# Kernel optimization log

Hardware: AMD Instinct MI355X
Metric: run time of the kernel (lower is better)

The kernel has to match this reference:

```python
import jax, jax.numpy as jnp
import numpy as np

B, C, H, W = 8, 256, 64, 64

def setup_inputs() -> dict:
    key = jax.random.key(0)
    ks = jax.random.split(key, 8)
    s = 0.02  # keep logits in a sane range
    return {
        "x": jax.random.normal(ks[0], (B, C, H, W), jnp.float32),
        "motion_info": jax.random.normal(ks[1], (B, C, H, W), jnp.float32),
        "wq": jax.random.normal(ks[2], (C, C), jnp.float32) * s,
        "bq": jax.random.normal(ks[3], (C,), jnp.float32) * s,
        "wk": jax.random.normal(ks[4], (C, C), jnp.float32) * s,
        "bk": jax.random.normal(ks[5], (C,), jnp.float32) * s,
        "wv": jax.random.normal(ks[6], (C, C), jnp.float32) * s,
        "bv": jax.random.normal(ks[7], (C,), jnp.float32) * s,
    }

def reference(x, motion_info, wq, bq, wk, bk, wv, bv):
    b, c, h, w = x.shape
    n = h * w
    scale = c ** (-0.5)
    # 1x1 convs == channel-mixing GEMMs; flatten spatial to tokens
    xf = x.reshape(b, c, n)              # [B,C,N]
    mf = motion_info.reshape(b, c, n)    # [B,C,N]
    q = jnp.einsum('dc,bcn->bdn', wq, xf) + bq[None, :, None]
    k = jnp.einsum('dc,bcn->bdn', wk, mf) + bk[None, :, None]
    v = jnp.einsum('dc,bcn->bdn', wv, mf) + bv[None, :, None]
    # attn[b,i,j] = <q[:,i], k[:,j]> * scale, softmax over j
    attn = jax.nn.softmax(jnp.einsum('bci,bcj->bij', q, k) * scale, axis=-1)
    # out[b,c,i] = sum_j v[b,c,j] * attn[b,i,j]
    out = jnp.einsum('bcj,bij->bci', v, attn)
    return out.reshape(b, c, h, w)
```

## Files before the change

kernel.cpp:

```cpp
#include <hip/hip_runtime.h>
#include <hip/hip_bf16.h>

#define BATCH 8
#define CH    256
#define NTOK  4096

typedef __bf16 bf16_t;
typedef __bf16 bf16x8 __attribute__((ext_vector_type(8)));
typedef __bf16 bf16x4 __attribute__((ext_vector_type(4)));
typedef float  fx4    __attribute__((ext_vector_type(4)));

#define GLOAD_LDS16(gptr, lptr) \
    __builtin_amdgcn_global_load_lds( \
        (const __attribute__((address_space(1))) void*)(gptr), \
        (__attribute__((address_space(3))) void*)(lptr), 16, 0, 0)


__global__ __launch_bounds__(256, 2) void proj_kernel(
    const float* __restrict__ x, const float* __restrict__ motion,
    const float* __restrict__ wq, const float* __restrict__ bq,
    const float* __restrict__ wk, const float* __restrict__ bk,
    const float* __restrict__ wv, const float* __restrict__ bv,
    bf16_t* __restrict__ qg, bf16_t* __restrict__ kg, bf16_t* __restrict__ vg)
{
    const int mat = blockIdx.y;
    const int b   = blockIdx.x & 7;
    const int n0  = (blockIdx.x >> 3) * 64;
    const float* __restrict__ src  = (mat == 0) ? x  : motion;
    const float* __restrict__ W    = (mat == 0) ? wq : (mat == 1 ? wk : wv);
    const float* __restrict__ bias = (mat == 0) ? bq : (mat == 1 ? bk : bv);

    __shared__ __align__(16) unsigned char smem[55296 + 1024];
    bf16_t* Xt    = (bf16_t*)smem;
    bf16_t* Wl    = (bf16_t*)(smem + 33792);
    bf16_t* OutL  = (bf16_t*)smem;
    float*  biasL = (float*)(smem + 55296);

    const int tid  = threadIdx.x;
    const int w    = tid >> 6;
    const int lane = tid & 63;
    const int l16  = lane & 15;
    const int quad = lane >> 4;

    biasL[tid] = bias[tid];

    for (int it = 0; it < 16; ++it) {
        const int c  = it * 16 + (tid >> 4);
        const int j4 = (tid & 15) * 4;
        const float4 v = *(const float4*)&src[((size_t)b * CH + c) * NTOK + n0 + j4];
        Xt[(j4 + 0) * 264 + c] = (bf16_t)v.x;
        Xt[(j4 + 1) * 264 + c] = (bf16_t)v.y;
        Xt[(j4 + 2) * 264 + c] = (bf16_t)v.z;
        Xt[(j4 + 3) * 264 + c] = (bf16_t)v.w;
    }

    fx4 acc[16];
    for (int i = 0; i < 16; ++i) acc[i] = (fx4){0.f, 0.f, 0.f, 0.f};

    for (int cs = 0; cs < 8; ++cs) {
        for (int it = 0; it < 8; ++it) {
            const int d  = it * 32 + (tid >> 3);
            const int c4 = (tid & 7) * 4;
            const float4 v = *(const float4*)&W[(size_t)d * CH + cs * 32 + c4];
            bf16x4 pk;
            pk[0] = (bf16_t)v.x; pk[1] = (bf16_t)v.y;
            pk[2] = (bf16_t)v.z; pk[3] = (bf16_t)v.w;
            *(bf16x4*)&Wl[d * 40 + c4] = pk;
        }
        __syncthreads();
        const bf16x8 af = *(const bf16x8*)&Xt[(w * 16 + l16) * 264 + cs * 32 + quad * 8];
        for (int dp = 0; dp < 16; ++dp) {
            const bf16x8 bf = *(const bf16x8*)&Wl[(dp * 16 + l16) * 40 + quad * 8];
            acc[dp] = __builtin_amdgcn_mfma_f32_16x16x32_bf16(af, bf, acc[dp], 0, 0, 0);
        }
        __syncthreads();
    }

    const float qs = (mat == 0) ? 0.0625f : 1.0f;
    for (int dp = 0; dp < 16; ++dp) {
        const int d = dp * 16 + l16;
        const float bb = biasL[d];
        bf16x4 pk;
        for (int r = 0; r < 4; ++r)
            pk[r] = (bf16_t)((acc[dp][r] + bb) * qs);
        *(bf16x4*)&OutL[d * 72 + w * 16 + quad * 4] = pk;
    }
    __syncthreads();

    if (mat < 2) {
        bf16_t* __restrict__ G = (mat == 0) ? qg : kg;
        for (int it = 0; it < 8; ++it) {
            const int n  = it * 8 + (tid >> 5);
            const int d8 = (tid & 31) * 8;
            bf16x8 vv;
            for (int k = 0; k < 8; ++k) vv[k] = OutL[(d8 + k) * 72 + n];
            *(bf16x8*)&G[((size_t)b * NTOK + n0 + n) * CH + d8] = vv;
        }
    } else {
        for (int it = 0; it < 8; ++it) {
            const int d  = it * 32 + (tid >> 3);
            const int n8 = (tid & 7) * 8;
            const bf16x8 vv = *(const bf16x8*)&OutL[d * 72 + n8];
            *(bf16x8*)&vg[((size_t)b * CH + d) * NTOK + n0 + n8] = vv;
        }
    }
}

__global__ __launch_bounds__(256, 2) void attn_kernel(
    const bf16_t* __restrict__ qg, const bf16_t* __restrict__ kg,
    const bf16_t* __restrict__ vg, float* __restrict__ out)
{
    const int b  = blockIdx.x & 7;
    const int i0 = (blockIdx.x >> 3) * 64;

    __shared__ __align__(16) unsigned char smem[54784];
    bf16_t* const K0   = (bf16_t*)smem;
    bf16_t* const K1   = (bf16_t*)(smem + 16384);
    bf16_t* const Vb   = (bf16_t*)(smem + 32768);
    bf16_t* const P    = (bf16_t*)(smem + 49152);
    float*  const lred = (float*)(smem + 54272);

    const int tid  = threadIdx.x;
    const int w    = tid >> 6;
    const int lane = tid & 63;
    const int l16  = lane & 15;
    const int quad = lane >> 4;
    const int ih   = w & 1;
    const int jh   = w >> 1;
    const int ch   = w & 1;
    const int is2  = w >> 1;
    const int w4   = w * 4;

    bf16x8 qf[2][8];
    #pragma unroll
    for (int isub = 0; isub < 2; ++isub) {
        const bf16_t* qb = qg + ((size_t)b * NTOK + i0 + ih * 32 + isub * 16 + l16) * CH;
        #pragma unroll
        for (int cs = 0; cs < 8; ++cs)
            qf[isub][cs] = *(const bf16x8*)(qb + cs * 32 + quad * 8);
    }

    fx4 oacc[8][2];
    #pragma unroll
    for (int i = 0; i < 8; ++i) {
        oacc[i][0] = (fx4){0.f, 0.f, 0.f, 0.f};
        oacc[i][1] = (fx4){0.f, 0.f, 0.f, 0.f};
    }
    float rs0[4] = {0.f, 0.f, 0.f, 0.f};
    float rs1[4] = {0.f, 0.f, 0.f, 0.f};

    const int jrow = jh * 16 + l16;
    const int sxk  = l16 & 7;
    const int svo  = (quad ^ (l16 & 3)) * 8;

    #pragma unroll
    for (int it = 0; it < 4; ++it) {
        const int N   = w4 + it;
        const int kj  = 2 * N + (lane >> 5);
        const int ksl = (lane & 31) ^ (kj & 7);
        GLOAD_LDS16(kg + (((size_t)b * NTOK + kj) << 8) + ksl * 8, K0 + N * 512);
    }
    __syncthreads();

    auto tile = [&](bf16_t* const Kc, bf16_t* const Kn, const int t) {
        const int j0 = t * 32;
        #pragma unroll
        for (int it = 0; it < 4; ++it) {
            const int N   = w4 + it;
            const int vc  = N * 16 + (lane >> 2);
            const int vsl = (lane & 3) ^ (vc & 3);
            GLOAD_LDS16(vg + (((size_t)b * CH + vc) << 12) + j0 + vsl * 8,
                        Vb + N * 512);
        }
        if (t + 1 < 128) {
            #pragma unroll
            for (int it = 0; it < 4; ++it) {
                const int N   = w4 + it;
                const int kj  = 2 * N + (lane >> 5);
                const int ksl = (lane & 31) ^ (kj & 7);
                GLOAD_LDS16(kg + (((size_t)b * NTOK + j0 + 32 + kj) << 8) + ksl * 8,
                            Kn + N * 512);
            }
        }

        fx4 s0 = (fx4){0.f, 0.f, 0.f, 0.f};
        fx4 s1 = (fx4){0.f, 0.f, 0.f, 0.f};
        {
            const bf16_t* krow = Kc + jrow * 256;
            #pragma unroll
            for (int cs = 0; cs < 8; ++cs) {
                const bf16x8 kf = *(const bf16x8*)(krow + (((cs * 4 + quad) ^ sxk) * 8));
                s0 = __builtin_amdgcn_mfma_f32_16x16x32_bf16(qf[0][cs], kf, s0, 0, 0, 0);
                s1 = __builtin_amdgcn_mfma_f32_16x16x32_bf16(qf[1][cs], kf, s1, 0, 0, 0);
            }
        }
        {
            bf16_t* prow = P + (ih * 32 + quad * 4) * 40 + jrow;
            #pragma unroll
            for (int r = 0; r < 4; ++r) {
                const float p0 = __expf(s0[r]);
                const float p1 = __expf(s1[r]);
                rs0[r] += p0;
                rs1[r] += p1;
                prow[r * 40]       = (bf16_t)p0;
                prow[r * 40 + 640] = (bf16_t)p1;
            }
        }
        __syncthreads();

        {
            const bf16x8 pf0 = *(const bf16x8*)(P + (is2 * 32 + l16) * 40 + quad * 8);
            const bf16x8 pf1 = *(const bf16x8*)(P + (is2 * 32 + 16 + l16) * 40 + quad * 8);
            const bf16_t* vbase = Vb + (ch * 128 + l16) * 32 + svo;
            #pragma unroll
            for (int cp8 = 0; cp8 < 8; ++cp8) {
                const bf16x8 vf = *(const bf16x8*)(vbase + cp8 * 512);
                oacc[cp8][0] = __builtin_amdgcn_mfma_f32_16x16x32_bf16(vf, pf0, oacc[cp8][0], 0, 0, 0);
                oacc[cp8][1] = __builtin_amdgcn_mfma_f32_16x16x32_bf16(vf, pf1, oacc[cp8][1], 0, 0, 0);
            }
        }
        __syncthreads();
    };

    #pragma unroll 1
    for (int t = 0; t < 128; t += 2) {
        tile(K0, K1, t);
        tile(K1, K0, t + 1);
    }

    #pragma unroll
    for (int r = 0; r < 4; ++r) {
        float v0 = rs0[r], v1 = rs1[r];
        v0 += __shfl_xor(v0, 1); v0 += __shfl_xor(v0, 2);
        v0 += __shfl_xor(v0, 4); v0 += __shfl_xor(v0, 8);
        v1 += __shfl_xor(v1, 1); v1 += __shfl_xor(v1, 2);
        v1 += __shfl_xor(v1, 4); v1 += __shfl_xor(v1, 8);
        rs0[r] = v0; rs1[r] = v1;
    }
    if (l16 == 0) {
        #pragma unroll
        for (int r = 0; r < 4; ++r) {
            lred[jh * 64 + ih * 32 + quad * 4 + r]      = rs0[r];
            lred[jh * 64 + ih * 32 + 16 + quad * 4 + r] = rs1[r];
        }
    }
    __syncthreads();

    const int   row0  = is2 * 32 + l16;
    const float linv0 = 1.0f / (lred[row0] + lred[64 + row0]);
    const float linv1 = 1.0f / (lred[row0 + 16] + lred[64 + row0 + 16]);

    const size_t obase = (size_t)b * CH * NTOK + i0 + is2 * 32 + l16;
    #pragma unroll
    for (int cp8 = 0; cp8 < 8; ++cp8) {
        const int c0 = (ch * 8 + cp8) * 16 + quad * 4;
        #pragma unroll
        for (int r = 0; r < 4; ++r) {
            out[obase + (size_t)(c0 + r) * NTOK]      = oacc[cp8][0][r] * linv0;
            out[obase + (size_t)(c0 + r) * NTOK + 16] = oacc[cp8][1][r] * linv1;
        }
    }
}

extern "C" void kernel_launch(void* const* d_in, const int* in_sizes, int n_in,
                              void* d_out, int out_size, void* d_ws, size_t ws_size,
                              hipStream_t stream) {
    const float* x  = (const float*)d_in[0];
    const float* mi = (const float*)d_in[1];
    const float* wq = (const float*)d_in[2];
    const float* bq = (const float*)d_in[3];
    const float* wk = (const float*)d_in[4];
    const float* bk = (const float*)d_in[5];
    const float* wv = (const float*)d_in[6];
    const float* bv = (const float*)d_in[7];

    bf16_t* qg = (bf16_t*)d_ws;
    bf16_t* kg = qg + (size_t)BATCH * NTOK * CH;
    bf16_t* vg = kg + (size_t)BATCH * NTOK * CH;

    dim3 pgrid(BATCH * (NTOK / 64), 3);
    proj_kernel<<<pgrid, 256, 0, stream>>>(x, mi, wq, bq, wk, bk, wv, bv, qg, kg, vg);
    attn_kernel<<<BATCH * (NTOK / 64), 256, 0, stream>>>(qg, kg, vg, (float*)d_out);
}
```

Baseline: 332.1 us.

## Pre-convert weights to bf16, register-resident projection, restructure attention pipeline

A new kernel converts the three weight matrices to bf16 once, using the output buffer as scratch. The projection kernel then keeps the X fragments in registers, reads the bf16 weights straight from global memory without LDS staging, swizzles Xt to avoid bank conflicts, and writes Q/K rows through a row-major LDS layout. The attention kernel switches from double-buffering K to double-buffering V, uses manual waitcnt/barrier placement with setprio around the MFMA loops, and packs P to bf16 in pairs via a lane shuffle. Together these aim to cut per-block weight conversion, LDS traffic and barrier stalls, at the cost of an extra launch and more fragile synchronisation.

```diff
diff --git a/kernel.cpp b/kernel.cpp
--- a/kernel.cpp
+++ b/kernel.cpp
@@ -16,25 +16,38 @@
         (__attribute__((address_space(3))) void*)(lptr), 16, 0, 0)
 
 
-__global__ __launch_bounds__(256, 2) void proj_kernel(
+__global__ __launch_bounds__(256) void wcvt_kernel(
+    const float* __restrict__ wq, const float* __restrict__ wk,
+    const float* __restrict__ wv, bf16_t* __restrict__ wb)
+{
+    const int mat = blockIdx.y;
+    const float* __restrict__ W = (mat == 0) ? wq : (mat == 1 ? wk : wv);
+    const int idx = (blockIdx.x * 256 + threadIdx.x) * 4;
+    const float4 v = *(const float4*)&W[idx];
+    bf16x4 pk;
+    pk[0] = (bf16_t)v.x; pk[1] = (bf16_t)v.y;
+    pk[2] = (bf16_t)v.z; pk[3] = (bf16_t)v.w;
+    *(bf16x4*)&wb[(size_t)mat * 65536 + idx] = pk;
+}
+
+__global__ __launch_bounds__(256, 3) void proj_kernel(
     const float* __restrict__ x, const float* __restrict__ motion,
-    const float* __restrict__ wq, const float* __restrict__ bq,
-    const float* __restrict__ wk, const float* __restrict__ bk,
-    const float* __restrict__ wv, const float* __restrict__ bv,
+    const bf16_t* __restrict__ wb,
+    const float* __restrict__ bq, const float* __restrict__ bk,
+    const float* __restrict__ bv,
     bf16_t* __restrict__ qg, bf16_t* __restrict__ kg, bf16_t* __restrict__ vg)
 {
     const int mat = blockIdx.y;
     const int b   = blockIdx.x & 7;
     const int n0  = (blockIdx.x >> 3) * 64;
-    const float* __restrict__ src  = (mat == 0) ? x  : motion;
-    const float* __restrict__ W    = (mat == 0) ? wq : (mat == 1 ? wk : wv);
+    const float* __restrict__ src  = (mat == 0) ? x : motion;
+    const bf16_t* __restrict__ W   = wb + (size_t)mat * 65536;
     const float* __restrict__ bias = (mat == 0) ? bq : (mat == 1 ? bk : bv);
 
-    __shared__ __align__(16) unsigned char smem[55296 + 1024];
+    __shared__ __align__(16) unsigned char smem[37888];
     bf16_t* Xt    = (bf16_t*)smem;
-    bf16_t* Wl    = (bf16_t*)(smem + 33792);
     bf16_t* OutL  = (bf16_t*)smem;
-    float*  biasL = (float*)(smem + 55296);
+    float*  biasL = (float*)(smem + 36864);
 
     const int tid  = threadIdx.x;
     const int w    = tid >> 6;
@@ -48,55 +61,73 @@
         const int c  = it * 16 + (tid >> 4);
         const int j4 = (tid & 15) * 4;
         const float4 v = *(const float4*)&src[((size_t)b * CH + c) * NTOK + n0 + j4];
-        Xt[(j4 + 0) * 264 + c] = (bf16_t)v.x;
-        Xt[(j4 + 1) * 264 + c] = (bf16_t)v.y;
-        Xt[(j4 + 2) * 264 + c] = (bf16_t)v.z;
-        Xt[(j4 + 3) * 264 + c] = (bf16_t)v.w;
+        const int g  = tid & 7;
+        const int pc = (((c >> 3) ^ g) << 3) + (c & 7);
+        Xt[(j4 + 0) * 264 + pc] = (bf16_t)v.x;
+        Xt[(j4 + 1) * 264 + pc] = (bf16_t)v.y;
+        Xt[(j4 + 2) * 264 + pc] = (bf16_t)v.z;
+        Xt[(j4 + 3) * 264 + pc] = (bf16_t)v.w;
+    }
+    __syncthreads();
+
+    bf16x8 af[8];
+    {
+        const int g = (4 * w + (l16 >> 2)) & 7;
+        const bf16_t* xr = Xt + (w * 16 + l16) * 264;
+        #pragma unroll
+        for (int cs = 0; cs < 8; ++cs)
+            af[cs] = *(const bf16x8*)(xr + (((cs * 4 + quad) ^ g) << 3));
     }
 
     fx4 acc[16];
+    #pragma unroll
     for (int i = 0; i < 16; ++i) acc[i] = (fx4){0.f, 0.f, 0.f, 0.f};
 
-    for (int cs = 0; cs < 8; ++cs) {
-        for (int it = 0; it < 8; ++it) {
-            const int d  = it * 32 + (tid >> 3);
-            const int c4 = (tid & 7) * 4;
-            const float4 v = *(const float4*)&W[(size_t)d * CH + cs * 32 + c4];
-            bf16x4 pk;
-            pk[0] = (bf16_t)v.x; pk[1] = (bf16_t)v.y;
-            pk[2] = (bf16_t)v.z; pk[3] = (bf16_t)v.w;
-            *(bf16x4*)&Wl[d * 40 + c4] = pk;
+    #pragma unroll 1
+    for (int dp = 0; dp < 16; ++dp) {
+        const bf16_t* wr = W + ((size_t)(dp * 16 + l16)) * 256 + quad * 8;
+        bf16x8 bfr[8];
+        #pragma unroll
+        for (int cs = 0; cs < 8; ++cs)
+            bfr[cs] = *(const bf16x8*)(wr + cs * 32);
+        #pragma unroll
+        for (int cs = 0; cs < 8; ++cs)
+            acc[dp] = __builtin_amdgcn_mfma_f32_16x16x32_bf16(af[cs], bfr[cs], acc[dp], 0, 0, 0);
+    }
+
+    __syncthreads();
+
+    const float qs = (mat == 0) ? 0.0625f : 1.0f;
+
+    if (mat < 2) {
+        #pragma unroll
+        for (int dp = 0; dp < 16; ++dp) {
+            const int d = dp * 16 + l16;
+            const float bb = biasL[d];
+            #pragma unroll
+            for (int r = 0; r < 4; ++r)
+                OutL[(w * 16 + quad * 4 + r) * 264 + d] = (bf16_t)((acc[dp][r] + bb) * qs);
         }
         __syncthreads();
-        const bf16x8 af = *(const bf16x8*)&Xt[(w * 16 + l16) * 264 + cs * 32 + quad * 8];
-        for (int dp = 0; dp < 16; ++dp) {
-            const bf16x8 bf = *(const bf16x8*)&Wl[(dp * 16 + l16) * 40 + quad * 8];
-            acc[dp] = __builtin_amdgcn_mfma_f32_16x16x32_bf16(af, bf, acc[dp], 0, 0, 0);
-        }
-        __syncthreads();
-    }
-
-    const float qs = (mat == 0) ? 0.0625f : 1.0f;
-    for (int dp = 0; dp < 16; ++dp) {
-        const int d = dp * 16 + l16;
-        const float bb = biasL[d];
-        bf16x4 pk;
-        for (int r = 0; r < 4; ++r)
-            pk[r] = (bf16_t)((acc[dp][r] + bb) * qs);
-        *(bf16x4*)&OutL[d * 72 + w * 16 + quad * 4] = pk;
-    }
-    __syncthreads();
-
-    if (mat < 2) {
         bf16_t* __restrict__ G = (mat == 0) ? qg : kg;
         for (int it = 0; it < 8; ++it) {
             const int n  = it * 8 + (tid >> 5);
             const int d8 = (tid & 31) * 8;
-            bf16x8 vv;
-            for (int k = 0; k < 8; ++k) vv[k] = OutL[(d8 + k) * 72 + n];
+            const bf16x8 vv = *(const bf16x8*)&OutL[n * 264 + d8];
             *(bf16x8*)&G[((size_t)b * NTOK + n0 + n) * CH + d8] = vv;
         }
     } else {
+        #pragma unroll
+        for (int dp = 0; dp < 16; ++dp) {
+            const int d = dp * 16 + l16;
+            const float bb = biasL[d];
+            bf16x4 pk;
+            #pragma unroll
+            for (int r = 0; r < 4; ++r)
+                pk[r] = (bf16_t)(acc[dp][r] + bb);
+            *(bf16x4*)&OutL[d * 72 + w * 16 + quad * 4] = pk;
+        }
+        __syncthreads();
         for (int it = 0; it < 8; ++it) {
             const int d  = it * 32 + (tid >> 3);
             const int n8 = (tid & 7) * 8;
@@ -114,9 +145,9 @@
     const int i0 = (blockIdx.x >> 3) * 64;
 
     __shared__ __align__(16) unsigned char smem[54784];
-    bf16_t* const K0   = (bf16_t*)smem;
-    bf16_t* const K1   = (bf16_t*)(smem + 16384);
-    bf16_t* const Vb   = (bf16_t*)(smem + 32768);
+    bf16_t* const Kb   = (bf16_t*)smem;
+    bf16_t* const V0   = (bf16_t*)(smem + 16384);
+    bf16_t* const V1   = (bf16_t*)(smem + 32768);
     bf16_t* const P    = (bf16_t*)(smem + 49152);
     float*  const lred = (float*)(smem + 54272);
 
@@ -151,81 +182,97 @@
 
     const int jrow = jh * 16 + l16;
     const int sxk  = l16 & 7;
-    const int svo  = (quad ^ (l16 & 3)) * 8;
-
-    #pragma unroll
-    for (int it = 0; it < 4; ++it) {
-        const int N   = w4 + it;
-        const int kj  = 2 * N + (lane >> 5);
-        const int ksl = (lane & 31) ^ (kj & 7);
-        GLOAD_LDS16(kg + (((size_t)b * NTOK + kj) << 8) + ksl * 8, K0 + N * 512);
-    }
-    __syncthreads();
-
-    auto tile = [&](bf16_t* const Kc, bf16_t* const Kn, const int t) {
+    const int svo  = (quad ^ ((l16 >> 1) & 3)) * 8;
+    const int vsl  = (lane & 3) ^ ((lane >> 3) & 3);
+
+    auto stageK = [&](int t) {
         const int j0 = t * 32;
         #pragma unroll
         for (int it = 0; it < 4; ++it) {
             const int N   = w4 + it;
-            const int vc  = N * 16 + (lane >> 2);
-            const int vsl = (lane & 3) ^ (vc & 3);
-            GLOAD_LDS16(vg + (((size_t)b * CH + vc) << 12) + j0 + vsl * 8,
-                        Vb + N * 512);
-        }
-        if (t + 1 < 128) {
-            #pragma unroll
-            for (int it = 0; it < 4; ++it) {
-                const int N   = w4 + it;
-                const int kj  = 2 * N + (lane >> 5);
-                const int ksl = (lane & 31) ^ (kj & 7);
-                GLOAD_LDS16(kg + (((size_t)b * NTOK + j0 + 32 + kj) << 8) + ksl * 8,
-                            Kn + N * 512);
-            }
-        }
+            const int kj  = 2 * N + (lane >> 5);
+            const int ksl = (lane & 31) ^ (kj & 7);
+            GLOAD_LDS16(kg + (((size_t)b * NTOK + j0 + kj) << 8) + ksl * 8, Kb + N * 512);
+        }
+    };
+    auto stageV = [&](bf16_t* Vb, int t) {
+        const int j0 = t * 32;
+        #pragma unroll
+        for (int it = 0; it < 4; ++it) {
+            const int N  = w4 + it;
+            const int vc = N * 16 + (lane >> 2);
+            GLOAD_LDS16(vg + (((size_t)b * CH + vc) << 12) + j0 + vsl * 8, Vb + N * 512);
+        }
+    };
+
+    stageK(0);
+    stageV(V0, 0);
+
+    auto tile = [&](bf16_t* const Vc, bf16_t* const Vn, const int t) {
+        asm volatile("s_waitcnt vmcnt(4)" ::: "memory");
+        __builtin_amdgcn_s_barrier();
+        __builtin_amdgcn_sched_barrier(0);
 
         fx4 s0 = (fx4){0.f, 0.f, 0.f, 0.f};
         fx4 s1 = (fx4){0.f, 0.f, 0.f, 0.f};
         {
-            const bf16_t* krow = Kc + jrow * 256;
+            const bf16_t* krow = Kb + jrow * 256;
+            __builtin_amdgcn_s_setprio(1);
             #pragma unroll
             for (int cs = 0; cs < 8; ++cs) {
                 const bf16x8 kf = *(const bf16x8*)(krow + (((cs * 4 + quad) ^ sxk) * 8));
                 s0 = __builtin_amdgcn_mfma_f32_16x16x32_bf16(qf[0][cs], kf, s0, 0, 0, 0);
                 s1 = __builtin_amdgcn_mfma_f32_16x16x32_bf16(qf[1][cs], kf, s1, 0, 0, 0);
             }
+            __builtin_amdgcn_s_setprio(0);
         }
         {
-            bf16_t* prow = P + (ih * 32 + quad * 4) * 40 + jrow;
+            bf16_t* prow = P + (ih * 32 + quad * 4) * 40 + jh * 16 + (l16 & ~1);
             #pragma unroll
             for (int r = 0; r < 4; ++r) {
                 const float p0 = __expf(s0[r]);
                 const float p1 = __expf(s1[r]);
                 rs0[r] += p0;
                 rs1[r] += p1;
-                prow[r * 40]       = (bf16_t)p0;
-                prow[r * 40 + 640] = (bf16_t)p1;
+                const float n0f = __shfl_xor(p0, 1);
+                const float n1f = __shfl_xor(p1, 1);
+                unsigned int pk0, pk1;
+                asm("v_cvt_pk_bf16_f32 %0, %1, %2" : "=v"(pk0) : "v"(p0), "v"(n0f));
+                asm("v_cvt_pk_bf16_f32 %0, %1, %2" : "=v"(pk1) : "v"(p1), "v"(n1f));
+                if (!(l16 & 1)) {
+                    *(unsigned int*)(prow + r * 40)       = pk0;
+                    *(unsigned int*)(prow + r * 40 + 640) = pk1;
+                }
             }
         }
-        __syncthreads();
+        asm volatile("s_waitcnt vmcnt(0) lgkmcnt(0)" ::: "memory");
+        __builtin_amdgcn_s_barrier();
+        __builtin_amdgcn_sched_barrier(0);
+
+        if (t + 1 < 128) {
+            stageK(t + 1);
+            stageV(Vn, t + 1);
+        }
 
         {
             const bf16x8 pf0 = *(const bf16x8*)(P + (is2 * 32 + l16) * 40 + quad * 8);
             const bf16x8 pf1 = *(const bf16x8*)(P + (is2 * 32 + 16 + l16) * 40 + quad * 8);
-            const bf16_t* vbase = Vb + (ch * 128 + l16) * 32 + svo;
+            const bf16_t* vbase = Vc + (ch * 128 + l16) * 32 + svo;
+            __builtin_amdgcn_s_setprio(1);
             #pragma unroll
             for (int cp8 = 0; cp8 < 8; ++cp8) {
                 const bf16x8 vf = *(const bf16x8*)(vbase + cp8 * 512);
                 oacc[cp8][0] = __builtin_amdgcn_mfma_f32_16x16x32_bf16(vf, pf0, oacc[cp8][0], 0, 0, 0);
                 oacc[cp8][1] = __builtin_amdgcn_mfma_f32_16x16x32_bf16(vf, pf1, oacc[cp8][1], 0, 0, 0);
             }
-        }
-        __syncthreads();
+            __builtin_amdgcn_s_setprio(0);
+        }
     };
 
     #pragma unroll 1
     for (int t = 0; t < 128; t += 2) {
-        tile(K0, K1, t);
-        tile(K1, K0, t + 1);
+        tile(V0, V1, t);
+        tile(V1, V0, t + 1);
     }
 
     #pragma unroll
@@ -237,6 +284,7 @@
         v1 += __shfl_xor(v1, 4); v1 += __shfl_xor(v1, 8);
         rs0[r] = v0; rs1[r] = v1;
     }
+    __syncthreads();
     if (l16 == 0) {
         #pragma unroll
         for (int r = 0; r < 4; ++r) {
@@ -277,8 +325,13 @@
     bf16_t* qg = (bf16_t*)d_ws;
     bf16_t* kg = qg + (size_t)BATCH * NTOK * CH;
     bf16_t* vg = kg + (size_t)BATCH * NTOK * CH;
+    bf16_t* wb = (bf16_t*)d_out;
+
+    dim3 wgrid(64, 3);
+    wcvt_kernel<<<wgrid, 256, 0, stream>>>(wq, wk, wv, wb);
 
     dim3 pgrid(BATCH * (NTOK / 64), 3);
-    proj_kernel<<<pgrid, 256, 0, stream>>>(x, mi, wq, bq, wk, bk, wv, bv, qg, kg, vg);
+    proj_kernel<<<pgrid, 256, 0, stream>>>(x, mi, wb, bq, bk, bv, qg, kg, vg);
+
     attn_kernel<<<BATCH * (NTOK / 64), 256, 0, stream>>>(qg, kg, vg, (float*)d_out);
 }
```

After: 433.9 us. 1.31x slower.
